# Optimization experiments

Measured on AMD Instinct MI355X. Metric: run time of the kernel, lower is better.

## Reference

```python
import jax, jax.numpy as jnp
from jax import lax
import numpy as np

VOCAB, EMB, H, T, B = 2500, 64, 64, 512, 256


def _gru_dir(x, mask, Wi, Wh, b, reverse):
    """Keras GRU (reset_after=True) over [B,T,D] with boolean mask [B,T].
    Masked steps carry state unchanged (Keras masking semantics; GRU output==state)."""
    bi, bh = b[0], b[1]
    if reverse:
        x = jnp.flip(x, 1)
        mask = jnp.flip(mask, 1)
    xp = x @ Wi + bi  # [B,T,3H], precompute input projections once

    def step(h, inp):
        xp_t, m_t = inp
        rec = h @ Wh + bh
        xz, xr, xh = jnp.split(xp_t, 3, axis=-1)
        rz, rr, rh = jnp.split(rec, 3, axis=-1)
        z = jax.nn.sigmoid(xz + rz)
        r = jax.nn.sigmoid(xr + rr)
        hh = jnp.tanh(xh + r * rh)
        h_new = z * h + (1.0 - z) * hh
        h = jnp.where(m_t, h_new, h)
        return h, h

    h0 = jnp.zeros((x.shape[0], Wh.shape[0]), x.dtype)
    hT, ys = lax.scan(step, h0, (jnp.swapaxes(xp, 0, 1), jnp.swapaxes(mask, 0, 1)[..., None]))
    ys = jnp.swapaxes(ys, 0, 1)  # [B,T,H]
    if reverse:
        ys = jnp.flip(ys, 1)
    return ys, hT


def _bigru_seq(x, mask, Wif, Whf, bf, Wib, Whb, bb):
    yf, _ = _gru_dir(x, mask, Wif, Whf, bf, False)
    yb, _ = _gru_dir(x, mask, Wib, Whb, bb, True)
    return jnp.concatenate([yf, yb], axis=-1)  # [B,T,2H]


def setup_inputs() -> dict:
    key = jax.random.key(0)
    ks = iter(jax.random.split(key, 40))
    s = 0.05
    d = {"tokens": jax.random.randint(next(ks), (B, T), 0, VOCAB)}
    d["emb"] = jax.random.normal(next(ks), (VOCAB, EMB), jnp.float32) * s
    for l, din in ((1, EMB), (2, 2 * H), (3, 2 * H)):
        for dr in ("f", "b"):
            d[f"wi{l}{dr}"] = jax.random.normal(next(ks), (din, 3 * H), jnp.float32) * s
            d[f"wh{l}{dr}"] = jax.random.normal(next(ks), (H, 3 * H), jnp.float32) * s
            d[f"bb{l}{dr}"] = jax.random.normal(next(ks), (2, 3 * H), jnp.float32) * s
    d["wd1"] = jax.random.normal(next(ks), (2 * H, 64), jnp.float32) * s
    d["bd1"] = jnp.zeros((64,), jnp.float32)
    d["wd2"] = jax.random.normal(next(ks), (64, 64), jnp.float32) * s
    d["bd2"] = jnp.zeros((64,), jnp.float32)
    d["wd3"] = jax.random.normal(next(ks), (64, 64), jnp.float32) * s
    d["bd3"] = jnp.zeros((64,), jnp.float32)
    d["wo"] = jax.random.normal(next(ks), (64, 28), jnp.float32) * s
    d["bo"] = jnp.zeros((28,), jnp.float32)
    return d


def reference(tokens, emb, wi1f, wh1f, bb1f, wi1b, wh1b, bb1b,
              wi2f, wh2f, bb2f, wi2b, wh2b, bb2b,
              wi3f, wh3f, bb3f, wi3b, wh3b, bb3b,
              wd1, bd1, wd2, bd2, wd3, bd3, wo, bo):
    mask = tokens > 0  # mask_zero=True
    x = emb[tokens]  # [B,T,EMB]
    x = _bigru_seq(x, mask, wi1f, wh1f, bb1f, wi1b, wh1b, bb1b)
    x = _bigru_seq(x, mask, wi2f, wh2f, bb2f, wi2b, wh2b, bb2b)
    _, hf = _gru_dir(x, mask, wi3f, wh3f, bb3f, False)
    _, hb = _gru_dir(x, mask, wi3b, wh3b, bb3b, True)
    x = jnp.concatenate([hf, hb], axis=-1)  # [B,2H]
    x = jax.nn.relu(x @ wd1 + bd1)
    x = jax.nn.relu(x @ wd2 + bd2)
    x = jax.nn.relu(x @ wd3 + bd3)
    return jax.nn.sigmoid(x @ wo + bo)  # [B,28]
```

## Files before the change

### kernel.cpp

```cpp
#include <hip/hip_runtime.h>
#include <hip/hip_bf16.h>
#include <cstddef>
#include <cstdint>

#define T_SEQ 512
#define BATCH 256
#define RTOT (BATCH * T_SEQ)
#define CHUNK 32
#define NCHUNK (T_SEQ / CHUNK)

__device__ __forceinline__ float fsigmoid(float x) {
    return 1.0f / (1.0f + __expf(-x));
}
__device__ __forceinline__ float ftanh(float x) {
    return 1.0f - 2.0f / (__expf(2.0f * x) + 1.0f);
}

template <int DIN, bool EMBED>
__global__ __launch_bounds__(192) void proj_kernel(
    const float* __restrict__ X, const int* __restrict__ tokens,
    const float* __restrict__ emb,
    const float* __restrict__ Wf, const float* __restrict__ bf_,
    const float* __restrict__ Wb, const float* __restrict__ bb_,
    float* __restrict__ xpf, float* __restrict__ xpb)
{
    constexpr int ROWS = 32;
    constexpr int PAD = 36;
    __shared__ __align__(16) float xt[DIN][PAD];
    const int r0 = blockIdx.x * ROWS;
    const int tid = threadIdx.x;

    for (int e = tid; e < ROWS * DIN; e += 192) {
        const int row = e / DIN;
        const int i = e % DIN;
        float v;
        if (EMBED) {
            v = emb[(size_t)tokens[r0 + row] * 64 + i];
        } else {
            v = X[(size_t)(r0 + row) * DIN + i];
        }
        xt[i][row] = v;
    }
    __syncthreads();

    const int col = tid;
    #pragma unroll
    for (int d = 0; d < 2; d++) {
        const float* __restrict__ W = d ? Wb : Wf;
        const float* __restrict__ bi = d ? bb_ : bf_;
        float* __restrict__ outp = d ? xpb : xpf;
        float acc[ROWS];
        const float b0 = bi[col];
        #pragma unroll
        for (int r = 0; r < ROWS; r++) acc[r] = b0;
        #pragma unroll 4
        for (int i = 0; i < DIN; i++) {
            const float w = W[i * 192 + col];
            #pragma unroll
            for (int r = 0; r < ROWS; r += 4) {
                const float4 x4 = *(const float4*)&xt[i][r];
                acc[r + 0] = fmaf(x4.x, w, acc[r + 0]);
                acc[r + 1] = fmaf(x4.y, w, acc[r + 1]);
                acc[r + 2] = fmaf(x4.z, w, acc[r + 2]);
                acc[r + 3] = fmaf(x4.w, w, acc[r + 3]);
            }
        }
        #pragma unroll
        for (int r = 0; r < ROWS; r++) {
            outp[(size_t)(r0 + r) * 192 + col] = acc[r];
        }
    }
}

__global__ __launch_bounds__(192) void gru_scan(
    const float* __restrict__ xpf, const float* __restrict__ xpb,
    const float* __restrict__ whf, const float* __restrict__ whb,
    const float* __restrict__ bbf, const float* __restrict__ bbb,
    const int* __restrict__ tokens,
    float* __restrict__ y,
    float* __restrict__ hfinal)
{
    const int chain = blockIdx.x;
    const int b = chain >> 1;
    const int dir = chain & 1;
    const float* __restrict__ xp = dir ? xpb : xpf;
    const float* __restrict__ wh = dir ? whb : whf;
    const float* __restrict__ bbp = dir ? bbb : bbf;
    const int k = threadIdx.x;
    const int j = k & 63;
    const int g = k >> 6;

    __shared__ __align__(16) float xbuf[2][CHUNK][192];
    __shared__ int   tok_lds[T_SEQ];
    __shared__ float zr[2][4][64];
    __shared__ __align__(16) float hw[3][2][64];

    float whk[64];
    #pragma unroll
    for (int i = 0; i < 64; i++) whk[i] = wh[i * 192 + k];
    const float bhk = bbp[192 + k];

    const size_t base = (size_t)b * T_SEQ;

    for (int i = k; i < T_SEQ; i += 192) tok_lds[i] = tokens[base + i];
    hw[g][0][j] = 0.0f;

    float4 stg[8];
    auto load_chunk = [&](int cc) {
        const int row_lo = dir ? (T_SEQ - CHUNK - cc * CHUNK) : (cc * CHUNK);
        const float4* gsrc = (const float4*)(xp + (base + row_lo) * 192);
        #pragma unroll
        for (int s = 0; s < 8; s++) stg[s] = gsrc[s * 192 + k];
    };
    auto write_chunk = [&](int cc) {
        float4* dst = (float4*)&xbuf[cc & 1][0][0];
        #pragma unroll
        for (int s = 0; s < 8; s++) dst[s * 192 + k] = stg[s];
    };

    load_chunk(0);
    write_chunk(0);
    __syncthreads();

    const int t0 = dir ? (T_SEQ - 1) : 0;
    const int st = dir ? -1 : 1;
    float hprev = 0.0f;
    float* yp = y ? (y + (base + t0) * 128 + (dir << 6) + j) : nullptr;
    const int ystep = st * 128;
    int te = t0;

    for (int c = 0; c < NCHUNK; c++) {
        const bool more = (c + 1 < NCHUNK);
        if (more) load_chunk(c + 1);
        const int pb = c & 1;
        #pragma unroll 2
        for (int tl = 0; tl < CHUNK; tl++) {
            const int t = c * CHUNK + tl;
            const int p = t & 1;
            const int tlp = dir ? (CHUNK - 1 - tl) : tl;

            const float xv = xbuf[pb][tlp][k];
            const int tok = tok_lds[te];

            float a0 = bhk, a1 = 0.0f, a2 = 0.0f, a3 = 0.0f;
            #pragma unroll
            for (int i = 0; i < 64; i += 4) {
                const float4 h4 = *(const float4*)&hw[g][p][i];
                a0 = fmaf(h4.x, whk[i + 0], a0);
                a1 = fmaf(h4.y, whk[i + 1], a1);
                a2 = fmaf(h4.z, whk[i + 2], a2);
                a3 = fmaf(h4.w, whk[i + 3], a3);
            }
            const float acc = (a0 + a1) + (a2 + a3);

            if (g == 0) {
                zr[p][0][j] = fsigmoid(xv + acc);
            } else if (g == 1) {
                zr[p][1][j] = fsigmoid(xv + acc);
            } else {
                zr[p][2][j] = acc;
                zr[p][3][j] = xv;
            }
            asm volatile("s_waitcnt lgkmcnt(0)" ::: "memory");
            __builtin_amdgcn_s_barrier();
            asm volatile("" ::: "memory");

            const float zg   = zr[p][0][j];
            const float rg   = zr[p][1][j];
            const float rech = zr[p][2][j];
            const float xh   = zr[p][3][j];
            const float cand = ftanh(xh + rg * rech);
            float hnew = zg * hprev + (1.0f - zg) * cand;
            if (!(tok > 0)) hnew = hprev;
            hw[g][p ^ 1][j] = hnew;
            if (g == 2 && yp) *yp = hnew;
            hprev = hnew;
            te += st;
            if (yp) yp += ystep;
        }
        if (more) write_chunk(c + 1);
        asm volatile("s_waitcnt lgkmcnt(0)" ::: "memory");
        __builtin_amdgcn_s_barrier();
        asm volatile("" ::: "memory");
    }
    if (hfinal && g == 2) {
        hfinal[b * 128 + (dir << 6) + j] = hprev;
    }
}

__global__ __launch_bounds__(64) void mlp_kernel(
    const float* __restrict__ hcat,
    const float* __restrict__ wd1, const float* __restrict__ bd1,
    const float* __restrict__ wd2, const float* __restrict__ bd2,
    const float* __restrict__ wd3, const float* __restrict__ bd3,
    const float* __restrict__ wo, const float* __restrict__ bo,
    float* __restrict__ outp)
{
    const int b = blockIdx.x;
    const int j = threadIdx.x;
    __shared__ float x0[128];
    __shared__ float x1[64];
    x0[j] = hcat[b * 128 + j];
    x0[j + 64] = hcat[b * 128 + 64 + j];
    __syncthreads();
    float a = bd1[j];
    #pragma unroll 4
    for (int i = 0; i < 128; i++) a = fmaf(x0[i], wd1[i * 64 + j], a);
    a = fmaxf(a, 0.0f);
    x1[j] = a;
    __syncthreads();
    float a2 = bd2[j];
    #pragma unroll 4
    for (int i = 0; i < 64; i++) a2 = fmaf(x1[i], wd2[i * 64 + j], a2);
    a2 = fmaxf(a2, 0.0f);
    __syncthreads();
    x1[j] = a2;
    __syncthreads();
    float a3 = bd3[j];
    #pragma unroll 4
    for (int i = 0; i < 64; i++) a3 = fmaf(x1[i], wd3[i * 64 + j], a3);
    a3 = fmaxf(a3, 0.0f);
    __syncthreads();
    x1[j] = a3;
    __syncthreads();
    if (j < 28) {
        float o = bo[j];
        #pragma unroll 4
        for (int i = 0; i < 64; i++) o = fmaf(x1[i], wo[i * 28 + j], o);
        outp[b * 28 + j] = fsigmoid(o);
    }
}

extern "C" void kernel_launch(void* const* d_in, const int* in_sizes, int n_in,
                              void* d_out, int out_size, void* d_ws, size_t ws_size,
                              hipStream_t stream)
{
    const int* tokens  = (const int*)d_in[0];
    const float* emb   = (const float*)d_in[1];
    const float* wi1f  = (const float*)d_in[2];
    const float* wh1f  = (const float*)d_in[3];
    const float* bb1f  = (const float*)d_in[4];
    const float* wi1b  = (const float*)d_in[5];
    const float* wh1b  = (const float*)d_in[6];
    const float* bb1b  = (const float*)d_in[7];
    const float* wi2f  = (const float*)d_in[8];
    const float* wh2f  = (const float*)d_in[9];
    const float* bb2f  = (const float*)d_in[10];
    const float* wi2b  = (const float*)d_in[11];
    const float* wh2b  = (const float*)d_in[12];
    const float* bb2b  = (const float*)d_in[13];
    const float* wi3f  = (const float*)d_in[14];
    const float* wh3f  = (const float*)d_in[15];
    const float* bb3f  = (const float*)d_in[16];
    const float* wi3b  = (const float*)d_in[17];
    const float* wh3b  = (const float*)d_in[18];
    const float* bb3b  = (const float*)d_in[19];
    const float* wd1   = (const float*)d_in[20];
    const float* bd1   = (const float*)d_in[21];
    const float* wd2   = (const float*)d_in[22];
    const float* bd2   = (const float*)d_in[23];
    const float* wd3   = (const float*)d_in[24];
    const float* bd3   = (const float*)d_in[25];
    const float* wo    = (const float*)d_in[26];
    const float* bo    = (const float*)d_in[27];

    float* y    = (float*)d_ws;
    float* xpf  = y + (size_t)RTOT * 128;
    float* xpb  = xpf + (size_t)RTOT * 192;
    float* hcat = y;

    const dim3 pb(192), pg(RTOT / 32);

    proj_kernel<64, true><<<pg, pb, 0, stream>>>(nullptr, tokens, emb,
                                                 wi1f, bb1f, wi1b, bb1b, xpf, xpb);
    gru_scan<<<512, 192, 0, stream>>>(xpf, xpb, wh1f, wh1b, bb1f, bb1b,
                                      tokens, y, nullptr);
    proj_kernel<128, false><<<pg, pb, 0, stream>>>(y, nullptr, nullptr,
                                                   wi2f, bb2f, wi2b, bb2b, xpf, xpb);
    gru_scan<<<512, 192, 0, stream>>>(xpf, xpb, wh2f, wh2b, bb2f, bb2b,
                                      tokens, y, nullptr);
    proj_kernel<128, false><<<pg, pb, 0, stream>>>(y, nullptr, nullptr,
                                                   wi3f, bb3f, wi3b, bb3b, xpf, xpb);
    gru_scan<<<512, 192, 0, stream>>>(xpf, xpb, wh3f, wh3b, bb3f, bb3b,
                                      tokens, nullptr, hcat);
    mlp_kernel<<<256, 64, 0, stream>>>(hcat, wd1, bd1, wd2, bd2, wd3, bd3,
                                       wo, bo, (float*)d_out);
}
```

Before: 1.705 ms.

## Process two batch chains per GRU block with readlane hidden broadcast and AGPR weights

```diff
diff --git a/kernel.cpp b/kernel.cpp
--- a/kernel.cpp
+++ b/kernel.cpp
@@ -72,7 +72,9 @@
     }
 }
 
-__global__ __launch_bounds__(192) void gru_scan(
+__global__ __launch_bounds__(192)
+__attribute__((amdgpu_waves_per_eu(1, 1)))
+void gru_scan(
     const float* __restrict__ xpf, const float* __restrict__ xpb,
     const float* __restrict__ whf, const float* __restrict__ whb,
     const float* __restrict__ bbf, const float* __restrict__ bbb,
@@ -80,111 +82,121 @@
     float* __restrict__ y,
     float* __restrict__ hfinal)
 {
-    const int chain = blockIdx.x;
-    const int b = chain >> 1;
-    const int dir = chain & 1;
-    const float* __restrict__ xp = dir ? xpb : xpf;
-    const float* __restrict__ wh = dir ? whb : whf;
-    const float* __restrict__ bbp = dir ? bbb : bbf;
+    const int blk = blockIdx.x;
+    const int dir = blk >> 7;
+    const int bp  = blk & 127;
+    const int bA = bp * 2, bB = bp * 2 + 1;
+    const float* __restrict__ xp  = dir ? xpb : xpf;
+    const float* __restrict__ wh  = dir ? whb : whf;
+    const float* __restrict__ bbp_ = dir ? bbb : bbf;
     const int k = threadIdx.x;
     const int j = k & 63;
     const int g = k >> 6;
 
-    __shared__ __align__(16) float xbuf[2][CHUNK][192];
-    __shared__ int   tok_lds[T_SEQ];
-    __shared__ float zr[2][4][64];
-    __shared__ __align__(16) float hw[3][2][64];
-
-    float whk[64];
+    __shared__ float zrs[2][8][64];
+    __shared__ __align__(16) float ybuf[2][CHUNK][64];
+    __shared__ int tokl[2][T_SEQ];
+
+    float wag[64];
     #pragma unroll
-    for (int i = 0; i < 64; i++) whk[i] = wh[i * 192 + k];
-    const float bhk = bbp[192 + k];
-
-    const size_t base = (size_t)b * T_SEQ;
-
-    for (int i = k; i < T_SEQ; i += 192) tok_lds[i] = tokens[base + i];
-    hw[g][0][j] = 0.0f;
-
-    float4 stg[8];
-    auto load_chunk = [&](int cc) {
-        const int row_lo = dir ? (T_SEQ - CHUNK - cc * CHUNK) : (cc * CHUNK);
-        const float4* gsrc = (const float4*)(xp + (base + row_lo) * 192);
-        #pragma unroll
-        for (int s = 0; s < 8; s++) stg[s] = gsrc[s * 192 + k];
-    };
-    auto write_chunk = [&](int cc) {
-        float4* dst = (float4*)&xbuf[cc & 1][0][0];
-        #pragma unroll
-        for (int s = 0; s < 8; s++) dst[s * 192 + k] = stg[s];
-    };
-
-    load_chunk(0);
-    write_chunk(0);
-    __syncthreads();
+    for (int i = 0; i < 64; i++) {
+        const float v = wh[i * 192 + k];
+        asm volatile("v_accvgpr_write_b32 %0, %1" : "=a"(wag[i]) : "v"(v));
+    }
+    const float bhk = bbp_[192 + k];
+
+    for (int i = k; i < T_SEQ; i += 192) {
+        tokl[0][i] = tokens[(size_t)bA * T_SEQ + i];
+        tokl[1][i] = tokens[(size_t)bB * T_SEQ + i];
+    }
 
     const int t0 = dir ? (T_SEQ - 1) : 0;
     const int st = dir ? -1 : 1;
-    float hprev = 0.0f;
-    float* yp = y ? (y + (base + t0) * 128 + (dir << 6) + j) : nullptr;
-    const int ystep = st * 128;
+    const size_t baseA = (size_t)bA * T_SEQ, baseB = (size_t)bB * T_SEQ;
+
+    float xA0 = xp[(baseA + t0) * 192 + k];
+    float xB0 = xp[(baseB + t0) * 192 + k];
+    float xA1 = xp[(baseA + t0 + st) * 192 + k];
+    float xB1 = xp[(baseB + t0 + st) * 192 + k];
+
+    float hA = 0.0f, hB = 0.0f;
+    __syncthreads();
+
     int te = t0;
-
     for (int c = 0; c < NCHUNK; c++) {
-        const bool more = (c + 1 < NCHUNK);
-        if (more) load_chunk(c + 1);
-        const int pb = c & 1;
-        #pragma unroll 2
         for (int tl = 0; tl < CHUNK; tl++) {
             const int t = c * CHUNK + tl;
             const int p = t & 1;
-            const int tlp = dir ? (CHUNK - 1 - tl) : tl;
-
-            const float xv = xbuf[pb][tlp][k];
-            const int tok = tok_lds[te];
-
-            float a0 = bhk, a1 = 0.0f, a2 = 0.0f, a3 = 0.0f;
+            const int tn = (t + 2 < T_SEQ) ? (t + 2) : (T_SEQ - 1);
+            const int te2 = t0 + st * tn;
+            const float xA2 = xp[(baseA + te2) * 192 + k];
+            const float xB2 = xp[(baseB + te2) * 192 + k];
+
+            float aA = bhk, aB = bhk;
+            const int hAb = __float_as_int(hA), hBb = __float_as_int(hB);
             #pragma unroll
-            for (int i = 0; i < 64; i += 4) {
-                const float4 h4 = *(const float4*)&hw[g][p][i];
-                a0 = fmaf(h4.x, whk[i + 0], a0);
-                a1 = fmaf(h4.y, whk[i + 1], a1);
-                a2 = fmaf(h4.z, whk[i + 2], a2);
-                a3 = fmaf(h4.w, whk[i + 3], a3);
-            }
-            const float acc = (a0 + a1) + (a2 + a3);
+            for (int i = 0; i < 64; i++) {
+                float w;
+                asm volatile("v_accvgpr_read_b32 %0, %1" : "=v"(w) : "a"(wag[i]));
+                const float hiA = __int_as_float(__builtin_amdgcn_readlane(hAb, i));
+                const float hiB = __int_as_float(__builtin_amdgcn_readlane(hBb, i));
+                aA = fmaf(hiA, w, aA);
+                aB = fmaf(hiB, w, aB);
+            }
 
             if (g == 0) {
-                zr[p][0][j] = fsigmoid(xv + acc);
+                zrs[p][0][j] = fsigmoid(xA0 + aA);
+                zrs[p][1][j] = fsigmoid(xB0 + aB);
             } else if (g == 1) {
-                zr[p][1][j] = fsigmoid(xv + acc);
+                zrs[p][2][j] = fsigmoid(xA0 + aA);
+                zrs[p][3][j] = fsigmoid(xB0 + aB);
             } else {
-                zr[p][2][j] = acc;
-                zr[p][3][j] = xv;
+                zrs[p][4][j] = aA;  zrs[p][5][j] = aB;
+                zrs[p][6][j] = xA0; zrs[p][7][j] = xB0;
             }
             asm volatile("s_waitcnt lgkmcnt(0)" ::: "memory");
             __builtin_amdgcn_s_barrier();
             asm volatile("" ::: "memory");
 
-            const float zg   = zr[p][0][j];
-            const float rg   = zr[p][1][j];
-            const float rech = zr[p][2][j];
-            const float xh   = zr[p][3][j];
-            const float cand = ftanh(xh + rg * rech);
-            float hnew = zg * hprev + (1.0f - zg) * cand;
-            if (!(tok > 0)) hnew = hprev;
-            hw[g][p ^ 1][j] = hnew;
-            if (g == 2 && yp) *yp = hnew;
-            hprev = hnew;
+            const float zA  = zrs[p][0][j], zB  = zrs[p][1][j];
+            const float rA  = zrs[p][2][j], rB  = zrs[p][3][j];
+            const float rhA = zrs[p][4][j], rhB = zrs[p][5][j];
+            const float xhA = zrs[p][6][j], xhB = zrs[p][7][j];
+            const float cA = ftanh(xhA + rA * rhA);
+            const float cB = ftanh(xhB + rB * rhB);
+            float nA = zA * hA + (1.0f - zA) * cA;
+            float nB = zB * hB + (1.0f - zB) * cB;
+            if (!(tokl[0][te] > 0)) nA = hA;
+            if (!(tokl[1][te] > 0)) nB = hB;
+            hA = nA; hB = nB;
+            if (g == 2 && y) {
+                ybuf[0][tl][j] = hA;
+                ybuf[1][tl][j] = hB;
+            }
             te += st;
-            if (yp) yp += ystep;
-        }
-        if (more) write_chunk(c + 1);
-        asm volatile("s_waitcnt lgkmcnt(0)" ::: "memory");
-        __builtin_amdgcn_s_barrier();
-        asm volatile("" ::: "memory");
+            xA0 = xA1; xA1 = xA2;
+            xB0 = xB1; xB1 = xB2;
+        }
+        if (y) {
+            asm volatile("s_waitcnt lgkmcnt(0)" ::: "memory");
+            __builtin_amdgcn_s_barrier();
+            asm volatile("" ::: "memory");
+            for (int idx = k; idx < 2 * CHUNK * 16; idx += 192) {
+                const int q   = idx & 15;
+                const int row = (idx >> 4) & (CHUNK - 1);
+                const int ch  = idx >> 9;
+                const int tt  = t0 + st * (c * CHUNK + row);
+                const size_t rb = (ch ? baseB : baseA) + tt;
+                const float4 v = *(const float4*)&ybuf[ch][row][q * 4];
+                *(float4*)&y[rb * 128 + (dir << 6) + q * 4] = v;
+            }
+            __builtin_amdgcn_s_barrier();
+            asm volatile("" ::: "memory");
+        }
     }
     if (hfinal && g == 2) {
-        hfinal[b * 128 + (dir << 6) + j] = hprev;
+        hfinal[bA * 128 + (dir << 6) + j] = hA;
+        hfinal[bB * 128 + (dir << 6) + j] = hB;
     }
 }
 
@@ -273,15 +285,15 @@
 
     proj_kernel<64, true><<<pg, pb, 0, stream>>>(nullptr, tokens, emb,
                                                  wi1f, bb1f, wi1b, bb1b, xpf, xpb);
-    gru_scan<<<512, 192, 0, stream>>>(xpf, xpb, wh1f, wh1b, bb1f, bb1b,
+    gru_scan<<<256, 192, 0, stream>>>(xpf, xpb, wh1f, wh1b, bb1f, bb1b,
                                       tokens, y, nullptr);
     proj_kernel<128, false><<<pg, pb, 0, stream>>>(y, nullptr, nullptr,
                                                    wi2f, bb2f, wi2b, bb2b, xpf, xpb);
-    gru_scan<<<512, 192, 0, stream>>>(xpf, xpb, wh2f, wh2b, bb2f, bb2b,
+    gru_scan<<<256, 192, 0, stream>>>(xpf, xpb, wh2f, wh2b, bb2f, bb2b,
                                       tokens, y, nullptr);
     proj_kernel<128, false><<<pg, pb, 0, stream>>>(y, nullptr, nullptr,
                                                    wi3f, bb3f, wi3b, bb3b, xpf, xpb);
-    gru_scan<<<512, 192, 0, stream>>>(xpf, xpb, wh3f, wh3b, bb3f, bb3b,
+    gru_scan<<<256, 192, 0, stream>>>(xpf, xpb, wh3f, wh3b, bb3f, bb3b,
                                       tokens, nullptr, hcat);
     mlp_kernel<<<256, 64, 0, stream>>>(hcat, wd1, bd1, wd2, bd2, wd3, bd3,
                                        wo, bo, (float*)d_out);
```

After: 2.421 ms. 42.0% more time.
